# Performance work log

Hardware: AMD Instinct MI355X
Metric: run time of the kernel (lower is better)

The kernel has to match this reference:

```python
import jax, jax.numpy as jnp
import numpy as np

N, F, P, O, E = 20000, 8, 12, 32, 320000


def setup_inputs() -> dict:
    key = jax.random.key(0)
    ks = jax.random.split(key, 18)
    g = lambda k, shape: (jax.random.normal(k, shape, jnp.float32) * 0.1)
    x = jax.random.normal(ks[0], (N, F, P), jnp.float32)
    edge_index = jax.random.randint(ks[1], (2, E), 0, N, dtype=jnp.int32)
    return {
        "x": x,
        "edge_index": edge_index,
        # GCNConv weights/biases for update (z), reset (r), candidate (h) gates
        "Wz": g(ks[2], (F, O)), "bz": g(ks[3], (O,)),
        "Wr": g(ks[4], (F, O)), "br": g(ks[5], (O,)),
        "Wh": g(ks[6], (F, O)), "bh": g(ks[7], (O,)),
        # GRU linear layers (torch.nn.Linear: y = x @ W.T + b), in=2*O, out=O
        "lz_w": g(ks[8], (O, 2 * O)), "lz_b": g(ks[9], (O,)),
        "lr_w": g(ks[10], (O, 2 * O)), "lr_b": g(ks[11], (O,)),
        "lh_w": g(ks[12], (O, 2 * O)), "lh_b": g(ks[13], (O,)),
        # temporal attention logits over periods
        "att": g(ks[14], (P,)),
        # final Linear(32 -> window_size)
        "out_w": g(ks[15], (P, O)), "out_b": g(ks[16], (P,)),
    }


def reference(x, edge_index, Wz, bz, Wr, br, Wh, bh,
              lz_w, lz_b, lr_w, lr_b, lh_w, lh_b, att, out_w, out_b):
    n = x.shape[0]
    # gcn_norm with self-loops: norm_e = d^-1/2[src] * d^-1/2[dst]
    loop = jnp.arange(n, dtype=edge_index.dtype)
    src = jnp.concatenate([edge_index[0], loop])
    dst = jnp.concatenate([edge_index[1], loop])
    deg = jax.ops.segment_sum(jnp.ones(src.shape[0], x.dtype), dst, num_segments=n)
    dinv = jnp.where(deg > 0, deg ** -0.5, 0.0)
    norm = dinv[src] * dinv[dst]  # [E+n]

    def gcn(xp, W, b):
        # xp: [n, P, F] -> [n, P, O]; GCNConv: D^-1/2 (A+I) D^-1/2 (X W) + b
        h = jnp.einsum('npf,fo->npo', xp, W)
        msg = h[src] * norm[:, None, None]  # [E+n, P, O]
        return jax.ops.segment_sum(msg, dst, num_segments=n) + b

    xp = jnp.transpose(x, (0, 2, 1))  # [n, P, F]
    # A3TGCN does NOT carry H across periods (H stays initial zeros), so all
    # periods are independent GRU steps from H = 0 and can be batched.
    H = jnp.zeros(xp.shape[:2] + (O,), x.dtype)
    Z = jax.nn.sigmoid(jnp.concatenate([gcn(xp, Wz, bz), H], -1) @ lz_w.T + lz_b)
    R = jax.nn.sigmoid(jnp.concatenate([gcn(xp, Wr, br), H], -1) @ lr_w.T + lr_b)
    Ht = jnp.tanh(jnp.concatenate([gcn(xp, Wh, bh), H * R], -1) @ lh_w.T + lh_b)
    Hp = Z * H + (1.0 - Z) * Ht  # [n, P, O]
    probs = jax.nn.softmax(att)
    Hacc = jnp.einsum('npo,p->no', Hp, probs)  # attention-weighted sum
    return jax.nn.relu(Hacc) @ out_w.T + out_b  # [n, window_size]
```

## Files before the change

### kernel.cpp

```cpp
#include <hip/hip_runtime.h>
#include <math.h>

#define FP 96
#define SLOT 64
#define NPB 16

__device__ __forceinline__ unsigned f2bf_bits(float f) {
    unsigned u = __float_as_uint(f);
    return (u + 0x7fffu + ((u >> 16) & 1u)) >> 16;
}
__device__ __forceinline__ float bf_lo(unsigned u) { return __uint_as_float(u << 16); }
__device__ __forceinline__ float bf_hi(unsigned u) { return __uint_as_float(u & 0xffff0000u); }

__global__ void k_histfill(const int* __restrict__ ei, int E,
                           int* __restrict__ cnt, int* __restrict__ bucket) {
    int e = blockIdx.x * blockDim.x + threadIdx.x;
    if (e >= E) return;
    int src = ei[e], dst = ei[E + e];
    int pos = atomicAdd(cnt + dst, 1);
    if (pos < SLOT) bucket[(size_t)dst * SLOT + pos] = src;
}

__global__ void k_prep(const float* __restrict__ Wz, const float* __restrict__ bz,
                       const float* __restrict__ Wh, const float* __restrict__ bh,
                       const float* __restrict__ lz_w, const float* __restrict__ lz_b,
                       const float* __restrict__ lh_w, const float* __restrict__ lh_b,
                       const float* __restrict__ att, const float* __restrict__ x,
                       const int* __restrict__ cnt,
                       float* __restrict__ cst, unsigned* __restrict__ xb, int N) {
    int b = blockIdx.x, t = threadIdx.x;
    if (b == 0) {
        int f = t >> 5, o = t & 31;
        float sz = 0.f, sh = 0.f;
        for (int j = 0; j < 32; ++j) {
            sz += Wz[f * 32 + j] * lz_w[o * 64 + j];
            sh += Wh[f * 32 + j] * lh_w[o * 64 + j];
        }
        cst[t]       = sz;
        cst[256 + t] = sh;
        if (t < 32) {
            float a = lz_b[t], c = lh_b[t];
            for (int j = 0; j < 32; ++j) {
                a += bz[j] * lz_w[t * 64 + j];
                c += bh[j] * lh_w[t * 64 + j];
            }
            cst[512 + t] = a;
            cst[544 + t] = c;
        }
        if (t < 12) {
            float m = -1e30f;
            for (int p = 0; p < 12; ++p) m = fmaxf(m, att[p]);
            float s = 0.f;
            for (int p = 0; p < 12; ++p) s += expf(att[p] - m);
            cst[576 + t] = expf(att[t] - m) / s;
        }
    } else {
        int i = (b - 1) * 256 + t;
        if (i < N * 12) {
            int n = i / 12;
            float w = rsqrtf((float)(cnt[n] + 1));
            const float4* x4 = (const float4*)x;
            float4 a = x4[i * 2], c = x4[i * 2 + 1];
            uint4 r;
            r.x = f2bf_bits(w * a.x) | (f2bf_bits(w * a.y) << 16);
            r.y = f2bf_bits(w * a.z) | (f2bf_bits(w * a.w) << 16);
            r.z = f2bf_bits(w * c.x) | (f2bf_bits(w * c.y) << 16);
            r.w = f2bf_bits(w * c.z) | (f2bf_bits(w * c.w) << 16);
            ((uint4*)xb)[i] = r;
        }
    }
}

__global__ void k_gather_gates(const unsigned* __restrict__ xb, const int* __restrict__ cnt,
                               const int* __restrict__ bucket, const float* __restrict__ cst,
                               const float* __restrict__ out_w, const float* __restrict__ out_b,
                               float* __restrict__ out, int N) {
    __shared__ float sy[NPB][FP + 4];
    __shared__ float shr[NPB][32];
    __shared__ float scst[588];
    int t = threadIdx.x;
    for (int i = t; i < 588; i += 256) scst[i] = cst[i];

    if (t < NPB * 12) {
        int nl = t / 12, k = t - nl * 12;
        int n = blockIdx.x * NPB + nl;
        if (n < N) {
            int c = cnt[n];
            int deg = min(c, SLOT);
            const int* bp = bucket + (size_t)n * SLOT;
            const uint4* xrow = (const uint4*)xb;
            uint4 v = xrow[n * 12 + k];
            float acc[8] = {bf_lo(v.x), bf_hi(v.x), bf_lo(v.y), bf_hi(v.y),
                            bf_lo(v.z), bf_hi(v.z), bf_lo(v.w), bf_hi(v.w)};
            int j = 0;
            for (; j + 4 <= deg; j += 4) {
                int4 s4 = *(const int4*)(bp + j);
                uint4 v0 = xrow[s4.x * 12 + k];
                uint4 v1 = xrow[s4.y * 12 + k];
                uint4 v2 = xrow[s4.z * 12 + k];
                uint4 v3 = xrow[s4.w * 12 + k];
                acc[0] += bf_lo(v0.x) + bf_lo(v1.x) + bf_lo(v2.x) + bf_lo(v3.x);
                acc[1] += bf_hi(v0.x) + bf_hi(v1.x) + bf_hi(v2.x) + bf_hi(v3.x);
                acc[2] += bf_lo(v0.y) + bf_lo(v1.y) + bf_lo(v2.y) + bf_lo(v3.y);
                acc[3] += bf_hi(v0.y) + bf_hi(v1.y) + bf_hi(v2.y) + bf_hi(v3.y);
                acc[4] += bf_lo(v0.z) + bf_lo(v1.z) + bf_lo(v2.z) + bf_lo(v3.z);
                acc[5] += bf_hi(v0.z) + bf_hi(v1.z) + bf_hi(v2.z) + bf_hi(v3.z);
                acc[6] += bf_lo(v0.w) + bf_lo(v1.w) + bf_lo(v2.w) + bf_lo(v3.w);
                acc[7] += bf_hi(v0.w) + bf_hi(v1.w) + bf_hi(v2.w) + bf_hi(v3.w);
            }
            for (; j < deg; ++j) {
                int s = bp[j];
                uint4 w = xrow[s * 12 + k];
                acc[0] += bf_lo(w.x); acc[1] += bf_hi(w.x);
                acc[2] += bf_lo(w.y); acc[3] += bf_hi(w.y);
                acc[4] += bf_lo(w.z); acc[5] += bf_hi(w.z);
                acc[6] += bf_lo(w.w); acc[7] += bf_hi(w.w);
            }
            float di = rsqrtf((float)(c + 1));
#pragma unroll
            for (int i = 0; i < 8; ++i) sy[nl][k * 8 + i] = di * acc[i];
        }
    }
    __syncthreads();

    int o = t & 31;
#pragma unroll
    for (int it = 0; it < 2; ++it) {
        int local = (t >> 5) + it * 8;
        int n = blockIdx.x * NPB + local;
        if (n < N) {
            const float* Mz = scst;
            const float* Mh = scst + 256;
            float cz = scst[512 + o], ch = scst[544 + o];
            float hacc = 0.f;
#pragma unroll
            for (int p = 0; p < 12; ++p) {
                float az = cz, ah = ch;
#pragma unroll
                for (int f = 0; f < 8; ++f) {
                    float xf = sy[local][f * 12 + p];
                    az += xf * Mz[f * 32 + o];
                    ah += xf * Mh[f * 32 + o];
                }
                float Z  = 1.f / (1.f + expf(-az));
                float Ht = tanhf(ah);
                hacc += scst[576 + p] * (1.f - Z) * Ht;
            }
            shr[local][o] = fmaxf(hacc, 0.f);
        }
    }
    __syncthreads();
#pragma unroll
    for (int it = 0; it < 2; ++it) {
        int local = (t >> 5) + it * 8;
        int n = blockIdx.x * NPB + local;
        if (n < N && o < 12) {
            float s = out_b[o];
#pragma unroll
            for (int j = 0; j < 32; ++j) s += shr[local][j] * out_w[o * 32 + j];
            out[(size_t)n * 12 + o] = s;
        }
    }
}

extern "C" void kernel_launch(void* const* d_in, const int* in_sizes, int n_in,
                              void* d_out, int out_size, void* d_ws, size_t ws_size,
                              hipStream_t stream) {
    const float* x    = (const float*)d_in[0];
    const int*   ei   = (const int*)d_in[1];
    const float* Wz   = (const float*)d_in[2];
    const float* bz   = (const float*)d_in[3];
    const float* Wh   = (const float*)d_in[6];
    const float* bh   = (const float*)d_in[7];
    const float* lz_w = (const float*)d_in[8];
    const float* lz_b = (const float*)d_in[9];
    const float* lh_w = (const float*)d_in[12];
    const float* lh_b = (const float*)d_in[13];
    const float* att  = (const float*)d_in[14];
    const float* ow   = (const float*)d_in[15];
    const float* ob   = (const float*)d_in[16];
    float* out = (float*)d_out;

    int N = in_sizes[0] / FP;
    int E = in_sizes[1] / 2;

    int*      cnt    = (int*)d_ws;
    int*      bucket = cnt + N;
    unsigned* xb     = (unsigned*)(bucket + (size_t)N * SLOT);
    float*    cst    = (float*)(xb + (size_t)N * 48);

    hipMemsetAsync(cnt, 0, (size_t)N * sizeof(int), stream);
    k_histfill<<<(E + 255) / 256, 256, 0, stream>>>(ei, E, cnt, bucket);
    int CB = (N * 12 + 255) / 256;
    k_prep    <<<1 + CB, 256, 0, stream>>>(Wz, bz, Wh, bh, lz_w, lz_b, lh_w, lh_b,
                                           att, x, cnt, cst, xb, N);
    k_gather_gates<<<(N + NPB - 1) / NPB, 256, 0, stream>>>(xb, cnt, bucket, cst, ow, ob, out, N);
}
```

Before: 163.7 us.

## Fold count reset into prep kernel and apply source normalization during gather

Replaces the memset with a count reset inside a new prep kernel that runs before the histogram. The bf16 conversion of x no longer depends on degree, so the source-side normalization is now applied in the gather by reading cnt of each neighbor. The gather kernel shrinks to 8 nodes per 128-thread block and stages neighbor indices, degrees and the transposed output weights in shared memory. This removes one launch and one pass's dependency on the histogram, at the cost of an extra scattered cnt load and rsqrt per edge in the gather loop.

```diff
diff --git a/kernel.cpp b/kernel.cpp
--- a/kernel.cpp
+++ b/kernel.cpp
@@ -3,7 +3,9 @@
 
 #define FP 96
 #define SLOT 64
-#define NPB 16
+#define NPB 8
+#define GBLK 128
+#define PBLK 256
 
 __device__ __forceinline__ unsigned f2bf_bits(float f) {
     unsigned u = __float_as_uint(f);
@@ -11,6 +13,60 @@
 }
 __device__ __forceinline__ float bf_lo(unsigned u) { return __uint_as_float(u << 16); }
 __device__ __forceinline__ float bf_hi(unsigned u) { return __uint_as_float(u & 0xffff0000u); }
+
+__global__ void k_pre(const float* __restrict__ Wz, const float* __restrict__ bz,
+                      const float* __restrict__ Wh, const float* __restrict__ bh,
+                      const float* __restrict__ lz_w, const float* __restrict__ lz_b,
+                      const float* __restrict__ lh_w, const float* __restrict__ lh_b,
+                      const float* __restrict__ att, const float* __restrict__ out_w,
+                      const float* __restrict__ out_b, const float* __restrict__ x,
+                      float* __restrict__ cst, int* __restrict__ cnt,
+                      unsigned* __restrict__ xb, int N) {
+    int b = blockIdx.x, t = threadIdx.x;
+    if (b == 0) {
+        int f = t >> 5, o = t & 31;
+        float sz = 0.f, sh = 0.f;
+        for (int j = 0; j < 32; ++j) {
+            sz += Wz[f * 32 + j] * lz_w[o * 64 + j];
+            sh += Wh[f * 32 + j] * lh_w[o * 64 + j];
+        }
+        cst[t]       = sz;
+        cst[256 + t] = sh;
+        if (t < 32) {
+            float a = lz_b[t], c = lh_b[t];
+            for (int j = 0; j < 32; ++j) {
+                a += bz[j] * lz_w[t * 64 + j];
+                c += bh[j] * lh_w[t * 64 + j];
+            }
+            cst[512 + t] = a;
+            cst[544 + t] = c;
+        }
+        if (t < 12) {
+            float m = -1e30f;
+            for (int p = 0; p < 12; ++p) m = fmaxf(m, att[p]);
+            float s = 0.f;
+            for (int p = 0; p < 12; ++p) s += expf(att[p] - m);
+            cst[576 + t] = expf(att[t] - m) / s;
+        }
+        for (int i = t; i < 384; i += PBLK)
+            cst[588 + (i & 31) * 12 + (i >> 5)] = out_w[i];
+        if (t < 12) cst[972 + t] = out_b[t];
+    } else {
+        int i = (b - 1) * PBLK + t;
+        if (i < N * 12) {
+            int n = i / 12;
+            if (i - n * 12 == 0) cnt[n] = 0;
+            const float4* x4 = (const float4*)x;
+            float4 a = x4[i * 2], c = x4[i * 2 + 1];
+            uint4 r;
+            r.x = f2bf_bits(a.x) | (f2bf_bits(a.y) << 16);
+            r.y = f2bf_bits(a.z) | (f2bf_bits(a.w) << 16);
+            r.z = f2bf_bits(c.x) | (f2bf_bits(c.y) << 16);
+            r.w = f2bf_bits(c.z) | (f2bf_bits(c.w) << 16);
+            ((uint4*)xb)[i] = r;
+        }
+    }
+}
 
 __global__ void k_histfill(const int* __restrict__ ei, int E,
                            int* __restrict__ cnt, int* __restrict__ bucket) {
@@ -21,102 +77,65 @@
     if (pos < SLOT) bucket[(size_t)dst * SLOT + pos] = src;
 }
 
-__global__ void k_prep(const float* __restrict__ Wz, const float* __restrict__ bz,
-                       const float* __restrict__ Wh, const float* __restrict__ bh,
-                       const float* __restrict__ lz_w, const float* __restrict__ lz_b,
-                       const float* __restrict__ lh_w, const float* __restrict__ lh_b,
-                       const float* __restrict__ att, const float* __restrict__ x,
-                       const int* __restrict__ cnt,
-                       float* __restrict__ cst, unsigned* __restrict__ xb, int N) {
-    int b = blockIdx.x, t = threadIdx.x;
-    if (b == 0) {
-        int f = t >> 5, o = t & 31;
-        float sz = 0.f, sh = 0.f;
-        for (int j = 0; j < 32; ++j) {
-            sz += Wz[f * 32 + j] * lz_w[o * 64 + j];
-            sh += Wh[f * 32 + j] * lh_w[o * 64 + j];
-        }
-        cst[t]       = sz;
-        cst[256 + t] = sh;
-        if (t < 32) {
-            float a = lz_b[t], c = lh_b[t];
-            for (int j = 0; j < 32; ++j) {
-                a += bz[j] * lz_w[t * 64 + j];
-                c += bh[j] * lh_w[t * 64 + j];
-            }
-            cst[512 + t] = a;
-            cst[544 + t] = c;
-        }
-        if (t < 12) {
-            float m = -1e30f;
-            for (int p = 0; p < 12; ++p) m = fmaxf(m, att[p]);
-            float s = 0.f;
-            for (int p = 0; p < 12; ++p) s += expf(att[p] - m);
-            cst[576 + t] = expf(att[t] - m) / s;
-        }
-    } else {
-        int i = (b - 1) * 256 + t;
-        if (i < N * 12) {
-            int n = i / 12;
-            float w = rsqrtf((float)(cnt[n] + 1));
-            const float4* x4 = (const float4*)x;
-            float4 a = x4[i * 2], c = x4[i * 2 + 1];
-            uint4 r;
-            r.x = f2bf_bits(w * a.x) | (f2bf_bits(w * a.y) << 16);
-            r.y = f2bf_bits(w * a.z) | (f2bf_bits(w * a.w) << 16);
-            r.z = f2bf_bits(w * c.x) | (f2bf_bits(w * c.y) << 16);
-            r.w = f2bf_bits(w * c.z) | (f2bf_bits(w * c.w) << 16);
-            ((uint4*)xb)[i] = r;
-        }
-    }
-}
-
-__global__ void k_gather_gates(const unsigned* __restrict__ xb, const int* __restrict__ cnt,
-                               const int* __restrict__ bucket, const float* __restrict__ cst,
-                               const float* __restrict__ out_w, const float* __restrict__ out_b,
-                               float* __restrict__ out, int N) {
+__global__ void __launch_bounds__(GBLK)
+k_gather_gates(const unsigned* __restrict__ xb, const int* __restrict__ cnt,
+               const int* __restrict__ bucket, const float* __restrict__ cst,
+               float* __restrict__ out, int N) {
     __shared__ float sy[NPB][FP + 4];
     __shared__ float shr[NPB][32];
-    __shared__ float scst[588];
+    __shared__ float scst[984];
+    __shared__ int   sbuck[NPB][68];
+    __shared__ int   sdeg[NPB];
     int t = threadIdx.x;
-    for (int i = t; i < 588; i += 256) scst[i] = cst[i];
-
+    for (int i = t; i < 984; i += GBLK) scst[i] = cst[i];
+
+    int n0 = blockIdx.x * NPB;
+    if (t < NPB) sdeg[t] = (n0 + t < N) ? cnt[n0 + t] : 0;
+    {
+        int nd = t >> 4, q = t & 15, n = n0 + nd;
+        if (n < N) *(int4*)&sbuck[nd][q * 4] =
+            ((const int4*)(bucket + (size_t)n * SLOT))[q];
+    }
+    __syncthreads();
+
+    const uint4* xrow = (const uint4*)xb;
     if (t < NPB * 12) {
-        int nl = t / 12, k = t - nl * 12;
-        int n = blockIdx.x * NPB + nl;
+        int nl = t / 12, k = t - nl * 12, n = n0 + nl;
         if (n < N) {
-            int c = cnt[n];
+            int c = sdeg[nl];
             int deg = min(c, SLOT);
-            const int* bp = bucket + (size_t)n * SLOT;
-            const uint4* xrow = (const uint4*)xb;
+            float di = rsqrtf((float)(c + 1));
             uint4 v = xrow[n * 12 + k];
-            float acc[8] = {bf_lo(v.x), bf_hi(v.x), bf_lo(v.y), bf_hi(v.y),
-                            bf_lo(v.z), bf_hi(v.z), bf_lo(v.w), bf_hi(v.w)};
+            float acc[8] = {di * bf_lo(v.x), di * bf_hi(v.x), di * bf_lo(v.y), di * bf_hi(v.y),
+                            di * bf_lo(v.z), di * bf_hi(v.z), di * bf_lo(v.w), di * bf_hi(v.w)};
             int j = 0;
             for (; j + 4 <= deg; j += 4) {
-                int4 s4 = *(const int4*)(bp + j);
-                uint4 v0 = xrow[s4.x * 12 + k];
-                uint4 v1 = xrow[s4.y * 12 + k];
-                uint4 v2 = xrow[s4.z * 12 + k];
-                uint4 v3 = xrow[s4.w * 12 + k];
-                acc[0] += bf_lo(v0.x) + bf_lo(v1.x) + bf_lo(v2.x) + bf_lo(v3.x);
-                acc[1] += bf_hi(v0.x) + bf_hi(v1.x) + bf_hi(v2.x) + bf_hi(v3.x);
-                acc[2] += bf_lo(v0.y) + bf_lo(v1.y) + bf_lo(v2.y) + bf_lo(v3.y);
-                acc[3] += bf_hi(v0.y) + bf_hi(v1.y) + bf_hi(v2.y) + bf_hi(v3.y);
-                acc[4] += bf_lo(v0.z) + bf_lo(v1.z) + bf_lo(v2.z) + bf_lo(v3.z);
-                acc[5] += bf_hi(v0.z) + bf_hi(v1.z) + bf_hi(v2.z) + bf_hi(v3.z);
-                acc[6] += bf_lo(v0.w) + bf_lo(v1.w) + bf_lo(v2.w) + bf_lo(v3.w);
-                acc[7] += bf_hi(v0.w) + bf_hi(v1.w) + bf_hi(v2.w) + bf_hi(v3.w);
+                int s0 = sbuck[nl][j],     s1 = sbuck[nl][j + 1];
+                int s2 = sbuck[nl][j + 2], s3 = sbuck[nl][j + 3];
+                uint4 v0 = xrow[s0 * 12 + k], v1 = xrow[s1 * 12 + k];
+                uint4 v2 = xrow[s2 * 12 + k], v3 = xrow[s3 * 12 + k];
+                float w0 = rsqrtf((float)(cnt[s0] + 1));
+                float w1 = rsqrtf((float)(cnt[s1] + 1));
+                float w2 = rsqrtf((float)(cnt[s2] + 1));
+                float w3 = rsqrtf((float)(cnt[s3] + 1));
+                acc[0] = fmaf(w0, bf_lo(v0.x), fmaf(w1, bf_lo(v1.x), fmaf(w2, bf_lo(v2.x), fmaf(w3, bf_lo(v3.x), acc[0]))));
+                acc[1] = fmaf(w0, bf_hi(v0.x), fmaf(w1, bf_hi(v1.x), fmaf(w2, bf_hi(v2.x), fmaf(w3, bf_hi(v3.x), acc[1]))));
+                acc[2] = fmaf(w0, bf_lo(v0.y), fmaf(w1, bf_lo(v1.y), fmaf(w2, bf_lo(v2.y), fmaf(w3, bf_lo(v3.y), acc[2]))));
+                acc[3] = fmaf(w0, bf_hi(v0.y), fmaf(w1, bf_hi(v1.y), fmaf(w2, bf_hi(v2.y), fmaf(w3, bf_hi(v3.y), acc[3]))));
+                acc[4] = fmaf(w0, bf_lo(v0.z), fmaf(w1, bf_lo(v1.z), fmaf(w2, bf_lo(v2.z), fmaf(w3, bf_lo(v3.z), acc[4]))));
+                acc[5] = fmaf(w0, bf_hi(v0.z), fmaf(w1, bf_hi(v1.z), fmaf(w2, bf_hi(v2.z), fmaf(w3, bf_hi(v3.z), acc[5]))));
+                acc[6] = fmaf(w0, bf_lo(v0.w), fmaf(w1, bf_lo(v1.w), fmaf(w2, bf_lo(v2.w), fmaf(w3, bf_lo(v3.w), acc[6]))));
+                acc[7] = fmaf(w0, bf_hi(v0.w), fmaf(w1, bf_hi(v1.w), fmaf(w2, bf_hi(v2.w), fmaf(w3, bf_hi(v3.w), acc[7]))));
             }
             for (; j < deg; ++j) {
-                int s = bp[j];
-                uint4 w = xrow[s * 12 + k];
-                acc[0] += bf_lo(w.x); acc[1] += bf_hi(w.x);
-                acc[2] += bf_lo(w.y); acc[3] += bf_hi(w.y);
-                acc[4] += bf_lo(w.z); acc[5] += bf_hi(w.z);
-                acc[6] += bf_lo(w.w); acc[7] += bf_hi(w.w);
-            }
-            float di = rsqrtf((float)(c + 1));
+                int s = sbuck[nl][j];
+                uint4 w4 = xrow[s * 12 + k];
+                float w = rsqrtf((float)(cnt[s] + 1));
+                acc[0] = fmaf(w, bf_lo(w4.x), acc[0]); acc[1] = fmaf(w, bf_hi(w4.x), acc[1]);
+                acc[2] = fmaf(w, bf_lo(w4.y), acc[2]); acc[3] = fmaf(w, bf_hi(w4.y), acc[3]);
+                acc[4] = fmaf(w, bf_lo(w4.z), acc[4]); acc[5] = fmaf(w, bf_hi(w4.z), acc[5]);
+                acc[6] = fmaf(w, bf_lo(w4.w), acc[6]); acc[7] = fmaf(w, bf_hi(w4.w), acc[7]);
+            }
 #pragma unroll
             for (int i = 0; i < 8; ++i) sy[nl][k * 8 + i] = di * acc[i];
         }
@@ -126,11 +145,8 @@
     int o = t & 31;
 #pragma unroll
     for (int it = 0; it < 2; ++it) {
-        int local = (t >> 5) + it * 8;
-        int n = blockIdx.x * NPB + local;
+        int local = (t >> 5) + it * 4, n = n0 + local;
         if (n < N) {
-            const float* Mz = scst;
-            const float* Mh = scst + 256;
             float cz = scst[512 + o], ch = scst[544 + o];
             float hacc = 0.f;
 #pragma unroll
@@ -139,8 +155,8 @@
 #pragma unroll
                 for (int f = 0; f < 8; ++f) {
                     float xf = sy[local][f * 12 + p];
-                    az += xf * Mz[f * 32 + o];
-                    ah += xf * Mh[f * 32 + o];
+                    az += xf * scst[f * 32 + o];
+                    ah += xf * scst[256 + f * 32 + o];
                 }
                 float Z  = 1.f / (1.f + expf(-az));
                 float Ht = tanhf(ah);
@@ -152,12 +168,12 @@
     __syncthreads();
 #pragma unroll
     for (int it = 0; it < 2; ++it) {
-        int local = (t >> 5) + it * 8;
-        int n = blockIdx.x * NPB + local;
+        int local = (t >> 5) + it * 4, n = n0 + local;
         if (n < N && o < 12) {
-            float s = out_b[o];
-#pragma unroll
-            for (int j = 0; j < 32; ++j) s += shr[local][j] * out_w[o * 32 + j];
+            float s = scst[972 + o];
+#pragma unroll
+            for (int j2 = 0; j2 < 32; ++j2)
+                s += shr[local][j2] * scst[588 + j2 * 12 + o];
             out[(size_t)n * 12 + o] = s;
         }
     }
@@ -189,10 +205,9 @@
     unsigned* xb     = (unsigned*)(bucket + (size_t)N * SLOT);
     float*    cst    = (float*)(xb + (size_t)N * 48);
 
-    hipMemsetAsync(cnt, 0, (size_t)N * sizeof(int), stream);
+    int CB = (N * 12 + PBLK - 1) / PBLK;
+    k_pre     <<<1 + CB, PBLK, 0, stream>>>(Wz, bz, Wh, bh, lz_w, lz_b, lh_w, lh_b,
+                                            att, ow, ob, x, cst, cnt, xb, N);
     k_histfill<<<(E + 255) / 256, 256, 0, stream>>>(ei, E, cnt, bucket);
-    int CB = (N * 12 + 255) / 256;
-    k_prep    <<<1 + CB, 256, 0, stream>>>(Wz, bz, Wh, bh, lz_w, lz_b, lh_w, lh_b,
-                                           att, x, cnt, cst, xb, N);
-    k_gather_gates<<<(N + NPB - 1) / NPB, 256, 0, stream>>>(xb, cnt, bucket, cst, ow, ob, out, N);
-}
+    k_gather_gates<<<(N + NPB - 1) / NPB, GBLK, 0, stream>>>(xb, cnt, bucket, cst, out, N);
+}
```

After: 145.1 us. -11.4%, faster.
